# Optimization experiments

Hardware: AMD Instinct MI355X
Metric: run time of the kernel (lower is better)

Reference implementation:

```python
import jax, jax.numpy as jnp
import numpy as np

DIM = 512
HEADS = 8
HD = DIM // HEADS
HIDDEN = 4 * DIM
EPS = 1e-5


def layernorm(x, g, b):
    mu = jnp.mean(x, axis=-1, keepdims=True)
    var = jnp.mean(jnp.square(x - mu), axis=-1, keepdims=True)
    return (x - mu) * jax.lax.rsqrt(var + EPS) * g + b


def setup_inputs() -> dict:
    key = jax.random.key(0)
    ks = jax.random.split(key, 10)
    B, P, N, C = 16, 4, 256, DIM
    s = 1.0 / np.sqrt(C)
    sh = 1.0 / np.sqrt(HIDDEN)
    return {
        "x": jax.random.normal(ks[0], (B, P, N, C), jnp.float32),
        "ln1_g": jnp.ones((C,), jnp.float32),
        "ln1_b": jnp.zeros((C,), jnp.float32),
        "w_qkv": jax.random.uniform(ks[1], (3 * C, C), jnp.float32, -s, s),
        "w_proj": jax.random.uniform(ks[2], (C, C), jnp.float32, -s, s),
        "b_proj": jax.random.uniform(ks[3], (C,), jnp.float32, -s, s),
        "ln2_g": jnp.ones((C,), jnp.float32),
        "ln2_b": jnp.zeros((C,), jnp.float32),
        "w1": jax.random.uniform(ks[4], (HIDDEN, C), jnp.float32, -s, s),
        "b1": jax.random.uniform(ks[5], (HIDDEN,), jnp.float32, -s, s),
        "w2": jax.random.uniform(ks[6], (C, HIDDEN), jnp.float32, -sh, sh),
        "b2": jax.random.uniform(ks[7], (C,), jnp.float32, -sh, sh),
    }


def reference(x, ln1_g, ln1_b, w_qkv, w_proj, b_proj, ln2_g, ln2_b, w1, b1, w2, b2):
    B, P, N, C = x.shape
    # --- attention branch (batched over B, P, heads; same math as the unrolled loops) ---
    h = layernorm(x, ln1_g, ln1_b)
    qkv = jnp.einsum('bpnc,dc->bpnd', h, w_qkv)            # [B,P,N,3C]
    qkv = qkv.reshape(B, P, N, 3, HEADS, HD)
    q, k, v = qkv[..., 0, :, :], qkv[..., 1, :, :], qkv[..., 2, :, :]  # [B,P,N,H,hd]
    scale = HD ** -0.5
    attn = jnp.einsum('bpnhd,bpmhd->bphnm', q * scale, k)  # [B,P,H,N,N]
    attn = jax.nn.softmax(attn, axis=-1)
    o = jnp.einsum('bphnm,bpmhd->bpnhd', attn, v).reshape(B, P, N, C)
    o = jnp.einsum('bpnc,dc->bpnd', o, w_proj) + b_proj
    x = x + o
    # --- MLP branch ---
    h = layernorm(x, ln2_g, ln2_b)
    h = jax.nn.gelu(jnp.einsum('bpnc,hc->bpnh', h, w1) + b1, approximate=False)
    h = jnp.einsum('bpnh,ch->bpnc', h, w2) + b2
    return x + h
```

## Files before the change

### kernel.cpp

```cpp
#include <hip/hip_runtime.h>

typedef __attribute__((ext_vector_type(8))) short short8;
typedef __attribute__((ext_vector_type(4))) float f32x4;
typedef __attribute__((ext_vector_type(2))) unsigned int u32x2;

__device__ __forceinline__ float bf2f(unsigned short u) {
    return __uint_as_float(((unsigned)u) << 16);
}
__device__ __forceinline__ unsigned short f2bf(float f) {
    unsigned u = __float_as_uint(f);
    u += 0x7fffu + ((u >> 16) & 1u);
    return (unsigned short)(u >> 16);
}
__device__ __forceinline__ unsigned pack2(float lo, float hi) {
    return (unsigned)f2bf(lo) | ((unsigned)f2bf(hi) << 16);
}
__device__ __forceinline__ void load_lds16(const void* g, void* l) {
    __builtin_amdgcn_global_load_lds(
        (const __attribute__((address_space(1))) void*)g,
        (__attribute__((address_space(3))) void*)l, 16, 0, 0);
}
__device__ __forceinline__ bool is_bf16(const unsigned* dt) {
    return *dt == 0x3F803F80u;
}
__device__ __forceinline__ float gelu_fast(float t) {
    float u = t * (0.7978845608f + 0.0356774081f * t * t);
    float e = __expf(-2.0f * fabsf(u));
    float th = (1.0f - e) / (1.0f + e);
    th = copysignf(th, u);
    return 0.5f * t * (1.0f + th);
}

__global__ __launch_bounds__(512) void cast_all(
    const void* s_wqkv, const void* s_wproj, const void* s_w1, const void* s_w2,
    const void* v0, const void* v1, const void* v2, const void* v3,
    const void* v4, const void* v5, const void* v6,
    unsigned short* d_wqkv, unsigned short* d_wproj, unsigned short* d_w1,
    unsigned short* d_w2, unsigned short* par, const unsigned* dt)
{
    bool isbf = is_bf16(dt);
    int b = blockIdx.x, tid = threadIdx.x;
    if (b < 768) {
        const void* src; unsigned short* dst; int off;
        if (b < 192)      { src = s_wqkv;  dst = d_wqkv;  off = b * 4096; }
        else if (b < 256) { src = s_wproj; dst = d_wproj; off = (b - 192) * 4096; }
        else if (b < 512) { src = s_w1;    dst = d_w1;    off = (b - 256) * 4096; }
        else              { src = s_w2;    dst = d_w2;    off = (b - 512) * 4096; }
        int i = off + tid * 8;
        if (isbf) {
            *(short8*)(dst + i) = *(const short8*)((const unsigned short*)src + i);
        } else {
            const float* s = (const float*)src + i;
            short8 o;
            #pragma unroll
            for (int j = 0; j < 8; ++j) o[j] = (short)f2bf(s[j]);
            *(short8*)(dst + i) = o;
        }
    } else {
        const void* srcs[7]  = {v0, v1, v2, v3, v4, v5, v6};
        const int   sizes[7] = {512, 512, 512, 512, 512, 2048, 512};
        const int   offs[7]  = {0, 512, 1024, 1536, 2048, 2560, 4608};
        int j = b - 768;
        const void* s = srcs[j];
        unsigned short* d = par + offs[j];
        for (int i = tid; i < sizes[j]; i += 512)
            d[i] = isbf ? ((const unsigned short*)s)[i] : f2bf(((const float*)s)[i]);
    }
}

__global__ __launch_bounds__(256) void ln_kernel(
    const void* __restrict__ xin, size_t row0,
    const unsigned* __restrict__ dt, int force_f32,
    const unsigned short* __restrict__ g, const unsigned short* __restrict__ b,
    unsigned short* __restrict__ y)
{
    int w = threadIdx.x >> 6, lane = threadIdx.x & 63;
    size_t lr = (size_t)blockIdx.x * 4 + w;
    size_t gr = row0 + lr;
    bool isf32 = force_f32 || !is_bf16(dt);
    float v[8];
    if (isf32) {
        const float* xr = (const float*)xin + (gr << 9) + (lane << 3);
        #pragma unroll
        for (int j = 0; j < 8; ++j) v[j] = xr[j];
    } else {
        short8 raw = *(const short8*)((const unsigned short*)xin + (gr << 9) + (lane << 3));
        #pragma unroll
        for (int j = 0; j < 8; ++j) v[j] = bf2f((unsigned short)raw[j]);
    }
    float sum = 0.f, sq = 0.f;
    #pragma unroll
    for (int j = 0; j < 8; ++j) { sum += v[j]; sq += v[j] * v[j]; }
    #pragma unroll
    for (int off = 32; off > 0; off >>= 1) {
        sum += __shfl_xor(sum, off);
        sq  += __shfl_xor(sq, off);
    }
    float mu  = sum * (1.0f / 512.0f);
    float var = sq * (1.0f / 512.0f) - mu * mu;
    float rs  = rsqrtf(var + 1e-5f);
    short8 gr8 = *(const short8*)(g + (lane << 3));
    short8 br8 = *(const short8*)(b + (lane << 3));
    short8 outv;
    #pragma unroll
    for (int j = 0; j < 8; ++j) {
        float o = (v[j] - mu) * rs * bf2f((unsigned short)gr8[j]) + bf2f((unsigned short)br8[j]);
        outv[j] = (short)f2bf(o);
    }
    *(short8*)(y + (lr << 9) + (lane << 3)) = outv;
}

template<int BM>
__global__ __launch_bounds__(256, (BM == 128) ? 4 : 2) void gemm6(
    const unsigned short* __restrict__ A, const unsigned short* __restrict__ W,
    const unsigned short* __restrict__ bias,
    const void* __restrict__ resid, size_t rrow0,
    void* __restrict__ out, size_t orow0,
    int NBY, int N, int K, int mode, const unsigned* __restrict__ dt)
{
    constexpr int BN = 128;
    constexpr int MJ = BM / 32;
    constexpr int AR = BM / 64;
    constexpr int BUFB = (BM + BN) * 64;
    constexpr int LDSZ = (2 * BUFB > BM * BN * 2) ? 2 * BUFB : BM * BN * 2;
    __shared__ char lds[LDSZ];

    int tid = threadIdx.x;
    int w = tid >> 6, lane = tid & 63;
    int l15 = lane & 15, g = lane >> 4;

    int L = blockIdx.x;
    int bx, by;
    if ((NBY & 7) == 0) {
        int nby8 = NBY >> 3;
        int xcd = L & 7, i = L >> 3;
        by = xcd * nby8 + (i % nby8);
        bx = i / nby8;
    } else {
        by = L % NBY;
        bx = L / NBY;
    }
    int m0 = by * BM, n0 = bx * BN;
    int wm = (BM == 256) ? ((w >> 1) << 7) : ((w >> 1) << 6);
    int wn = (w & 1) << 6;

    int srow_t = ((tid >> 3) << 1) | (tid & 1);
    int u_t = ((tid >> 1) & 3) ^ ((tid >> 3) & 3);
    const unsigned short* gA[AR];
    const unsigned short* gB[2];
    #pragma unroll
    for (int j = 0; j < AR; ++j)
        gA[j] = A + (size_t)(m0 + j * 64 + srow_t) * K + u_t * 8;
    #pragma unroll
    for (int j = 0; j < 2; ++j)
        gB[j] = W + (size_t)(n0 + j * 64 + srow_t) * K + u_t * 8;
    int lslot = tid * 16;

    int off = (l15 >> 1) * 128 + ((g ^ ((l15 >> 1) & 3)) << 5) + ((l15 & 1) << 4);

    f32x4 acc[4][MJ];
    #pragma unroll
    for (int i = 0; i < 4; ++i)
        #pragma unroll
        for (int j = 0; j < MJ; ++j) acc[i][j] = (f32x4){0.f, 0.f, 0.f, 0.f};

    #pragma unroll
    for (int j = 0; j < AR; ++j)
        load_lds16(gA[j], &lds[j * 4096 + lslot]);
    #pragma unroll
    for (int j = 0; j < 2; ++j)
        load_lds16(gB[j], &lds[BM * 64 + j * 4096 + lslot]);

    int p = 0;
    for (int k = 0; k < K; k += 32) {
        __syncthreads();
        if (k + 32 < K) {
            int kn = k + 32;
            char* nb = &lds[(p ^ 1) * BUFB];
            #pragma unroll
            for (int j = 0; j < AR; ++j)
                load_lds16(gA[j] + kn, nb + j * 4096 + lslot);
            #pragma unroll
            for (int j = 0; j < 2; ++j)
                load_lds16(gB[j] + kn, nb + BM * 64 + j * 4096 + lslot);
        }
        const char* bAct = &lds[p * BUFB];
        const char* bW = bAct + BM * 64;
        short8 wf[4], af[MJ];
        #pragma unroll
        for (int i = 0; i < 4; ++i)
            wf[i] = *(const short8*)(bW + (wn + i * 16) * 64 + off);
        #pragma unroll
        for (int j = 0; j < MJ; ++j)
            af[j] = *(const short8*)(bAct + (wm + j * 16) * 64 + off);
        #pragma unroll
        for (int i = 0; i < 4; ++i)
            #pragma unroll
            for (int j = 0; j < MJ; ++j)
                acc[i][j] = __builtin_amdgcn_mfma_f32_16x16x32_bf16(wf[i], af[j], acc[i][j], 0, 0, 0);
        p ^= 1;
    }

    char* tb = (char*)lds;
    __syncthreads();
    #pragma unroll
    for (int j = 0; j < MJ; ++j) {
        int mloc = wm + j * 16 + l15;
        char* rowp = tb + mloc * (BN * 2);
        int sw = mloc & (BN / 4 - 2);
        #pragma unroll
        for (int i = 0; i < 4; ++i) {
            int cq = (wn + i * 16 + g * 4) >> 2;
            u32x2 pk = {pack2(acc[i][j][0], acc[i][j][1]),
                        pack2(acc[i][j][2], acc[i][j][3])};
            *(u32x2*)(rowp + ((cq ^ sw) << 3)) = pk;
        }
    }
    __syncthreads();

    int rL = tid >> 4;
    int lc = tid & 15;
    bool inbf = is_bf16(dt);
    int colg = n0 + lc * 8;
    float bv[8];
    if (bias) {
        short8 bb = *(const short8*)(bias + colg);
        #pragma unroll
        for (int t = 0; t < 8; ++t) bv[t] = bf2f((unsigned short)bb[t]);
    } else {
        #pragma unroll
        for (int t = 0; t < 8; ++t) bv[t] = 0.f;
    }

    #pragma unroll 4
    for (int ps = 0; ps < BM / 16; ++ps) {
        int row = ps * 16 + rL;
        int rowL = m0 + row;
        int c16 = lc ^ ((row >> 1) & 15);
        short8 vv = *(const short8*)(tb + row * (BN * 2) + (c16 << 4));
        float vals[8];
        #pragma unroll
        for (int t = 0; t < 8; ++t) vals[t] = bf2f((unsigned short)vv[t]) + bv[t];

        if (mode == 0) {
            *(short8*)((unsigned short*)out + (size_t)rowL * N + colg) = vv;
        } else if (mode == 2) {
            short8 ov;
            #pragma unroll
            for (int t = 0; t < 8; ++t) ov[t] = (short)f2bf(gelu_fast(vals[t]));
            *(short8*)((unsigned short*)out + (size_t)rowL * N + colg) = ov;
        } else if (mode == 1) {
            size_t rbase = (rrow0 + rowL) * (size_t)N + colg;
            float o8[8];
            if (inbf) {
                short8 rr = *(const short8*)((const unsigned short*)resid + rbase);
                #pragma unroll
                for (int t = 0; t < 8; ++t) o8[t] = bf2f((unsigned short)rr[t]) + vals[t];
            } else {
                f32x4 r0 = *(const f32x4*)((const float*)resid + rbase);
                f32x4 r1 = *(const f32x4*)((const float*)resid + rbase + 4);
                #pragma unroll
                for (int t = 0; t < 4; ++t) { o8[t] = r0[t] + vals[t]; o8[t + 4] = r1[t] + vals[t + 4]; }
            }
            float* ob = (float*)out + (size_t)rowL * N + colg;
            *(f32x4*)ob       = (f32x4){o8[0], o8[1], o8[2], o8[3]};
            *(f32x4*)(ob + 4) = (f32x4){o8[4], o8[5], o8[6], o8[7]};
        } else {
            size_t rbase = (size_t)rowL * N + colg;
            f32x4 r0 = *(const f32x4*)((const float*)resid + rbase);
            f32x4 r1 = *(const f32x4*)((const float*)resid + rbase + 4);
            float o8[8];
            #pragma unroll
            for (int t = 0; t < 4; ++t) { o8[t] = r0[t] + vals[t]; o8[t + 4] = r1[t] + vals[t + 4]; }
            size_t obase = (orow0 + rowL) * (size_t)N + colg;
            if (inbf) {
                short8 ov;
                #pragma unroll
                for (int t = 0; t < 8; ++t) ov[t] = (short)f2bf(o8[t]);
                *(short8*)((unsigned short*)out + obase) = ov;
            } else {
                float* ob = (float*)out + obase;
                *(f32x4*)ob       = (f32x4){o8[0], o8[1], o8[2], o8[3]};
                *(f32x4*)(ob + 4) = (f32x4){o8[4], o8[5], o8[6], o8[7]};
            }
        }
    }
}

__global__ __launch_bounds__(256) void attn_mfma(
    const unsigned short* __restrict__ qkv, unsigned short* __restrict__ o)
{
    __shared__ unsigned short Vt[64 * 256];
    __shared__ unsigned short Ps[4][16 * 256];
    int bp = blockIdx.x >> 3, h = blockIdx.x & 7;
    const unsigned short* base = qkv + (size_t)bp * 256 * 1536;
    int qo = h << 6, ko = 512 + (h << 6), vo = 1024 + (h << 6);
    int tid = threadIdx.x, w = tid >> 6, lane = tid & 63;
    int l15 = lane & 15, g = lane >> 4;

    {
        int d = tid & 63;
        for (int s = tid >> 6; s < 256; s += 4) {
            unsigned short v = base[(size_t)s * 1536 + vo + d];
            *(unsigned short*)((char*)Vt + d * 512 + (((s >> 3) ^ (d & 7)) << 4) + ((s & 7) << 1)) = v;
        }
    }
    __syncthreads();

    unsigned short* P = Ps[w];

    for (int pass = 0; pass < 4; ++pass) {
        int q0 = pass * 64 + w * 16;
        short8 qa[2];
        #pragma unroll
        for (int t = 0; t < 2; ++t)
            qa[t] = *(const short8*)(base + (size_t)(q0 + l15) * 1536 + qo + t * 32 + g * 8);
        f32x4 S[16];
        #pragma unroll
        for (int ns = 0; ns < 16; ++ns) {
            f32x4 a = {0.f, 0.f, 0.f, 0.f};
            #pragma unroll
            for (int t = 0; t < 2; ++t) {
                short8 kb = *(const short8*)(base + (size_t)(ns * 16 + l15) * 1536 + ko + t * 32 + g * 8);
                a = __builtin_amdgcn_mfma_f32_16x16x32_bf16(qa[t], kb, a, 0, 0, 0);
            }
            S[ns] = a;
        }
        float mx[4], sums[4], inv[4];
        #pragma unroll
        for (int r = 0; r < 4; ++r) {
            float m = -1e30f;
            #pragma unroll
            for (int ns = 0; ns < 16; ++ns) m = fmaxf(m, S[ns][r]);
            m *= 0.125f;
            #pragma unroll
            for (int off = 1; off < 16; off <<= 1) m = fmaxf(m, __shfl_xor(m, off));
            mx[r] = m;
            sums[r] = 0.f;
        }
        #pragma unroll
        for (int ns = 0; ns < 16; ++ns)
            #pragma unroll
            for (int r = 0; r < 4; ++r) {
                float p = __expf(S[ns][r] * 0.125f - mx[r]);
                sums[r] += p;
                S[ns][r] = p;
            }
        #pragma unroll
        for (int r = 0; r < 4; ++r) {
            float s2 = sums[r];
            #pragma unroll
            for (int off = 1; off < 16; off <<= 1) s2 += __shfl_xor(s2, off);
            inv[r] = 1.0f / s2;
        }
        #pragma unroll
        for (int ns = 0; ns < 16; ++ns)
            #pragma unroll
            for (int r = 0; r < 4; ++r) {
                int mq = g * 4 + r;
                int s = ns * 16 + l15;
                *(unsigned short*)((char*)P + mq * 512 + (((s >> 3) ^ (mq & 7)) << 4) + ((s & 7) << 1))
                    = f2bf(S[ns][r] * inv[r]);
            }
        f32x4 O[4];
        #pragma unroll
        for (int ds = 0; ds < 4; ++ds) O[ds] = (f32x4){0.f, 0.f, 0.f, 0.f};
        #pragma unroll
        for (int ks = 0; ks < 8; ++ks) {
            int c = (ks * 4 + g) ^ (l15 & 7);
            short8 pa = *(const short8*)((const char*)P + l15 * 512 + (c << 4));
            #pragma unroll
            for (int ds = 0; ds < 4; ++ds) {
                short8 vb = *(const short8*)((const char*)Vt + (ds * 16 + l15) * 512 + (c << 4));
                O[ds] = __builtin_amdgcn_mfma_f32_16x16x32_bf16(pa, vb, O[ds], 0, 0, 0);
            }
        }
        #pragma unroll
        for (int ds = 0; ds < 4; ++ds)
            #pragma unroll
            for (int r = 0; r < 4; ++r) {
                int mq = q0 + g * 4 + r;
                int d = ds * 16 + l15;
                o[((size_t)(bp * 256 + mq) << 9) + (h << 6) + d] = f2bf(O[ds][r]);
            }
    }
}

extern "C" void kernel_launch(void* const* d_in, const int* in_sizes, int n_in,
                              void* d_out, int out_size, void* d_ws, size_t ws_size,
                              hipStream_t stream)
{
    const void* x      = d_in[0];
    const void* ln1_g  = d_in[1];
    const void* ln1_b  = d_in[2];
    const void* w_qkv  = d_in[3];
    const void* w_proj = d_in[4];
    const void* b_proj = d_in[5];
    const void* ln2_g  = d_in[6];
    const void* ln2_b  = d_in[7];
    const void* w1     = d_in[8];
    const void* b1     = d_in[9];
    const void* w2     = d_in[10];
    const void* b2     = d_in[11];
    const unsigned* dt = (const unsigned*)ln1_g;

    const int M = 16384;
    char* ws = (char*)d_ws;
    unsigned short* wqkv_b  = (unsigned short*)(ws);
    unsigned short* wproj_b = (unsigned short*)(ws + 1572864);
    unsigned short* w1_b    = (unsigned short*)(ws + 2097152);
    unsigned short* w2_b    = (unsigned short*)(ws + 4194304);
    unsigned short* par     = (unsigned short*)(ws + 6291456);
    const size_t CAST_END = 6308096;

    unsigned short* p_g1    = par + 0;
    unsigned short* p_b1ln  = par + 512;
    unsigned short* p_bproj = par + 1024;
    unsigned short* p_g2    = par + 1536;
    unsigned short* p_b2ln  = par + 2048;
    unsigned short* p_b1    = par + 2560;
    unsigned short* p_b2    = par + 4608;

    int NC = 64;
    const int cand[7] = {1, 2, 4, 8, 16, 32, 64};
    for (int i = 0; i < 7; ++i) {
        size_t need = CAST_END + (size_t)(M / cand[i]) * 11264;
        if (need <= ws_size) { NC = cand[i]; break; }
    }
    const int R = M / NC;

    char* cb = ws + CAST_END;
    unsigned short* h   = (unsigned short*)(cb);
    unsigned short* qkv = (unsigned short*)(cb + (size_t)R * 1024);
    unsigned short* o   = (unsigned short*)(cb + (size_t)R * 4096);
    float*          x2  = (float*)        (cb + (size_t)R * 5120);
    unsigned short* hid = (unsigned short*)(cb + (size_t)R * 7168);
    unsigned short* h2  = h;

    cast_all<<<775, 512, 0, stream>>>(w_qkv, w_proj, w1, w2,
                                      ln1_g, ln1_b, b_proj, ln2_g, ln2_b, b1, b2,
                                      wqkv_b, wproj_b, w1_b, w2_b, par, dt);

    for (int c = 0; c < NC; ++c) {
        const size_t r0 = (size_t)c * R;

        ln_kernel<<<R / 4, 256, 0, stream>>>(x, r0, dt, 0, p_g1, p_b1ln, h);
        gemm6<256><<<(1536 / 128) * (R / 256), 256, 0, stream>>>(
            h, wqkv_b, nullptr, nullptr, 0, qkv, 0, R / 256, 1536, 512, 0, dt);
        attn_mfma<<<(R / 256) * 8, 256, 0, stream>>>(qkv, o);
        gemm6<128><<<(512 / 128) * (R / 128), 256, 0, stream>>>(
            o, wproj_b, p_bproj, x, r0, x2, 0, R / 128, 512, 512, 1, dt);
        ln_kernel<<<R / 4, 256, 0, stream>>>(x2, 0, dt, 1, p_g2, p_b2ln, h2);
        gemm6<256><<<(2048 / 128) * (R / 256), 256, 0, stream>>>(
            h2, w1_b, p_b1, nullptr, 0, hid, 0, R / 256, 2048, 512, 2, dt);
        gemm6<128><<<(512 / 128) * (R / 128), 256, 0, stream>>>(
            hid, w2_b, p_b2, x2, 0, d_out, r0, R / 128, 512, 2048, 3, dt);
    }
}
```

Baseline: 336.4 us.

## Replace LDS-staged GEMM with direct global-to-register MFMA fragment loads

Result: slower. 545.5 us (+62.2%).

```diff
diff --git a/kernel.cpp b/kernel.cpp
--- a/kernel.cpp
+++ b/kernel.cpp
@@ -14,11 +14,6 @@
 }
 __device__ __forceinline__ unsigned pack2(float lo, float hi) {
     return (unsigned)f2bf(lo) | ((unsigned)f2bf(hi) << 16);
-}
-__device__ __forceinline__ void load_lds16(const void* g, void* l) {
-    __builtin_amdgcn_global_load_lds(
-        (const __attribute__((address_space(1))) void*)g,
-        (__attribute__((address_space(3))) void*)l, 16, 0, 0);
 }
 __device__ __forceinline__ bool is_bf16(const unsigned* dt) {
     return *dt == 0x3F803F80u;
@@ -110,8 +105,7 @@
     *(short8*)(y + (lr << 9) + (lane << 3)) = outv;
 }
 
-template<int BM>
-__global__ __launch_bounds__(256, (BM == 128) ? 4 : 2) void gemm6(
+__global__ __launch_bounds__(256, 3) void gemm7(
     const unsigned short* __restrict__ A, const unsigned short* __restrict__ W,
     const unsigned short* __restrict__ bias,
     const void* __restrict__ resid, size_t rrow0,
@@ -119,11 +113,7 @@
     int NBY, int N, int K, int mode, const unsigned* __restrict__ dt)
 {
     constexpr int BN = 128;
-    constexpr int MJ = BM / 32;
-    constexpr int AR = BM / 64;
-    constexpr int BUFB = (BM + BN) * 64;
-    constexpr int LDSZ = (2 * BUFB > BM * BN * 2) ? 2 * BUFB : BM * BN * 2;
-    __shared__ char lds[LDSZ];
+    __shared__ char tb[128 * BN * 2];
 
     int tid = threadIdx.x;
     int w = tid >> 6, lane = tid & 63;
@@ -140,71 +130,56 @@
         by = L % NBY;
         bx = L / NBY;
     }
-    int m0 = by * BM, n0 = bx * BN;
-    int wm = (BM == 256) ? ((w >> 1) << 7) : ((w >> 1) << 6);
+    int m0 = by << 7, n0 = bx << 7;
+    int wm = (w >> 1) << 6;
     int wn = (w & 1) << 6;
 
-    int srow_t = ((tid >> 3) << 1) | (tid & 1);
-    int u_t = ((tid >> 1) & 3) ^ ((tid >> 3) & 3);
-    const unsigned short* gA[AR];
-    const unsigned short* gB[2];
-    #pragma unroll
-    for (int j = 0; j < AR; ++j)
-        gA[j] = A + (size_t)(m0 + j * 64 + srow_t) * K + u_t * 8;
-    #pragma unroll
-    for (int j = 0; j < 2; ++j)
-        gB[j] = W + (size_t)(n0 + j * 64 + srow_t) * K + u_t * 8;
-    int lslot = tid * 16;
-
-    int off = (l15 >> 1) * 128 + ((g ^ ((l15 >> 1) & 3)) << 5) + ((l15 & 1) << 4);
-
-    f32x4 acc[4][MJ];
+    const unsigned short* wp[4];
+    const unsigned short* ap[4];
     #pragma unroll
     for (int i = 0; i < 4; ++i)
-        #pragma unroll
-        for (int j = 0; j < MJ; ++j) acc[i][j] = (f32x4){0.f, 0.f, 0.f, 0.f};
-
-    #pragma unroll
-    for (int j = 0; j < AR; ++j)
-        load_lds16(gA[j], &lds[j * 4096 + lslot]);
-    #pragma unroll
-    for (int j = 0; j < 2; ++j)
-        load_lds16(gB[j], &lds[BM * 64 + j * 4096 + lslot]);
-
-    int p = 0;
-    for (int k = 0; k < K; k += 32) {
-        __syncthreads();
-        if (k + 32 < K) {
-            int kn = k + 32;
-            char* nb = &lds[(p ^ 1) * BUFB];
-            #pragma unroll
-            for (int j = 0; j < AR; ++j)
-                load_lds16(gA[j] + kn, nb + j * 4096 + lslot);
-            #pragma unroll
-            for (int j = 0; j < 2; ++j)
-                load_lds16(gB[j] + kn, nb + BM * 64 + j * 4096 + lslot);
-        }
-        const char* bAct = &lds[p * BUFB];
-        const char* bW = bAct + BM * 64;
-        short8 wf[4], af[MJ];
+        wp[i] = W + (size_t)(n0 + wn + i * 16 + l15) * K + g * 8;
+    #pragma unroll
+    for (int j = 0; j < 4; ++j)
+        ap[j] = A + (size_t)(m0 + wm + j * 16 + l15) * K + g * 8;
+
+    f32x4 acc[4][4];
+    #pragma unroll
+    for (int i = 0; i < 4; ++i)
+        #pragma unroll
+        for (int j = 0; j < 4; ++j) acc[i][j] = (f32x4){0.f, 0.f, 0.f, 0.f};
+
+    short8 wf0[4], af0[4], wf1[4], af1[4];
+    #pragma unroll
+    for (int i = 0; i < 4; ++i) wf0[i] = *(const short8*)(wp[i]);
+    #pragma unroll
+    for (int j = 0; j < 4; ++j) af0[j] = *(const short8*)(ap[j]);
+
+    for (int k = 0; k < K; k += 64) {
+        #pragma unroll
+        for (int i = 0; i < 4; ++i) wf1[i] = *(const short8*)(wp[i] + k + 32);
+        #pragma unroll
+        for (int j = 0; j < 4; ++j) af1[j] = *(const short8*)(ap[j] + k + 32);
         #pragma unroll
         for (int i = 0; i < 4; ++i)
-            wf[i] = *(const short8*)(bW + (wn + i * 16) * 64 + off);
-        #pragma unroll
-        for (int j = 0; j < MJ; ++j)
-            af[j] = *(const short8*)(bAct + (wm + j * 16) * 64 + off);
+            #pragma unroll
+            for (int j = 0; j < 4; ++j)
+                acc[i][j] = __builtin_amdgcn_mfma_f32_16x16x32_bf16(wf0[i], af0[j], acc[i][j], 0, 0, 0);
+        if (k + 64 < K) {
+            #pragma unroll
+            for (int i = 0; i < 4; ++i) wf0[i] = *(const short8*)(wp[i] + k + 64);
+            #pragma unroll
+            for (int j = 0; j < 4; ++j) af0[j] = *(const short8*)(ap[j] + k + 64);
+        }
         #pragma unroll
         for (int i = 0; i < 4; ++i)
             #pragma unroll
-            for (int j = 0; j < MJ; ++j)
-                acc[i][j] = __builtin_amdgcn_mfma_f32_16x16x32_bf16(wf[i], af[j], acc[i][j], 0, 0, 0);
-        p ^= 1;
-    }
-
-    char* tb = (char*)lds;
-    __syncthreads();
-    #pragma unroll
-    for (int j = 0; j < MJ; ++j) {
+            for (int j = 0; j < 4; ++j)
+                acc[i][j] = __builtin_amdgcn_mfma_f32_16x16x32_bf16(wf1[i], af1[j], acc[i][j], 0, 0, 0);
+    }
+
+    #pragma unroll
+    for (int j = 0; j < 4; ++j) {
         int mloc = wm + j * 16 + l15;
         char* rowp = tb + mloc * (BN * 2);
         int sw = mloc & (BN / 4 - 2);
@@ -233,7 +208,7 @@
     }
 
     #pragma unroll 4
-    for (int ps = 0; ps < BM / 16; ++ps) {
+    for (int ps = 0; ps < 8; ++ps) {
         int row = ps * 16 + rL;
         int rowL = m0 + row;
         int c16 = lc ^ ((row >> 1) & 15);
@@ -443,17 +418,18 @@
 
     for (int c = 0; c < NC; ++c) {
         const size_t r0 = (size_t)c * R;
+        const int NBY = R / 128;
 
         ln_kernel<<<R / 4, 256, 0, stream>>>(x, r0, dt, 0, p_g1, p_b1ln, h);
-        gemm6<256><<<(1536 / 128) * (R / 256), 256, 0, stream>>>(
-            h, wqkv_b, nullptr, nullptr, 0, qkv, 0, R / 256, 1536, 512, 0, dt);
+        gemm7<<<(1536 / 128) * NBY, 256, 0, stream>>>(
+            h, wqkv_b, nullptr, nullptr, 0, qkv, 0, NBY, 1536, 512, 0, dt);
         attn_mfma<<<(R / 256) * 8, 256, 0, stream>>>(qkv, o);
-        gemm6<128><<<(512 / 128) * (R / 128), 256, 0, stream>>>(
-            o, wproj_b, p_bproj, x, r0, x2, 0, R / 128, 512, 512, 1, dt);
+        gemm7<<<(512 / 128) * NBY, 256, 0, stream>>>(
+            o, wproj_b, p_bproj, x, r0, x2, 0, NBY, 512, 512, 1, dt);
         ln_kernel<<<R / 4, 256, 0, stream>>>(x2, 0, dt, 1, p_g2, p_b2ln, h2);
-        gemm6<256><<<(2048 / 128) * (R / 256), 256, 0, stream>>>(
-            h2, w1_b, p_b1, nullptr, 0, hid, 0, R / 256, 2048, 512, 2, dt);
-        gemm6<128><<<(512 / 128) * (R / 128), 256, 0, stream>>>(
-            hid, w2_b, p_b2, x2, 0, d_out, r0, R / 128, 512, 2048, 3, dt);
-    }
-}
+        gemm7<<<(2048 / 128) * NBY, 256, 0, stream>>>(
+            h2, w1_b, p_b1, nullptr, 0, hid, 0, NBY, 2048, 512, 2, dt);
+        gemm7<<<(512 / 128) * NBY, 256, 0, stream>>>(
+            hid, w2_b, p_b2, x2, 0, d_out, r0, NBY, 512, 2048, 3, dt);
+    }
+}
```
